# Kernel tuning notes

Hardware: AMD Instinct MI355X
Metric: run time of the kernel (lower is better)

Reference implementation:

```python
import jax, jax.numpy as jnp
import numpy as np

INPUT_DIM = 128
HIDDEN_DIM = 128
WINDOW_SIZE = 256
BLOCK_SIZE = 256
BATCH = 8
SEQ = 8192


def setup_inputs() -> dict:
    key = jax.random.key(0)
    ks = jax.random.split(key, 7)
    s = 1.0 / np.sqrt(INPUT_DIM)
    return {
        "x": jax.random.normal(ks[0], (BATCH, SEQ, INPUT_DIM), dtype=jnp.float32),
        "Wq": jax.random.normal(ks[1], (HIDDEN_DIM, INPUT_DIM), dtype=jnp.float32) * s,
        "bq": jax.random.normal(ks[2], (HIDDEN_DIM,), dtype=jnp.float32) * s,
        "Wk": jax.random.normal(ks[3], (HIDDEN_DIM, INPUT_DIM), dtype=jnp.float32) * s,
        "bk": jax.random.normal(ks[4], (HIDDEN_DIM,), dtype=jnp.float32) * s,
        "Wv": jax.random.normal(ks[5], (HIDDEN_DIM, INPUT_DIM), dtype=jnp.float32) * s,
        "bv": jax.random.normal(ks[6], (HIDDEN_DIM,), dtype=jnp.float32) * s,
    }


def reference(x, Wq, bq, Wk, bk, Wv, bv):
    B, S, D = x.shape
    bs, w = BLOCK_SIZE, WINDOW_SIZE
    nb = S // bs
    halo = w - 1
    W = bs + 2 * halo  # per-block K/V window width

    q = x @ Wq.T + bq  # [B,S,H]
    k = x @ Wk.T + bk
    v = x @ Wv.T + bv

    # Zero-pad K/V by halo on both sides. Since there is NO softmax, padded
    # zero keys give zero scores and padded zero values contribute zero —
    # this exactly reproduces the torch code's clamped window slicing.
    k_pad = jnp.pad(k, ((0, 0), (halo, halo), (0, 0)))
    v_pad = jnp.pad(v, ((0, 0), (halo, halo), (0, 0)))

    # Gather overlapping windows: [B, nb, W, H]
    starts = jnp.arange(nb) * bs  # window start in padded coords
    idx = starts[:, None] + jnp.arange(W)[None, :]  # [nb, W]
    k_win = k_pad[:, idx, :]
    v_win = v_pad[:, idx, :]

    q_blk = q.reshape(B, nb, bs, -1)  # [B, nb, bs, H]

    scale = 1.0 / jnp.sqrt(jnp.float32(D))
    attn = jnp.einsum('bnqh,bnkh->bnqk', q_blk, k_win) * scale  # no softmax
    out = jnp.einsum('bnqk,bnkh->bnqh', attn, v_win)
    return out.reshape(B, S, -1)
```

## Files before the change

kernel.cpp:

```cpp
#include <hip/hip_runtime.h>
#include <stdint.h>


#define B_ 8
#define S_ 8192
#define LDT 68
#define LDG 164
#define LDM 132
#define LDQP 36
#define XTB 21760
#define GOFF 43520
#define SMEMSZ 96000

using bf16x4 = __attribute__((ext_vector_type(4))) short;
using bf16x8 = __attribute__((ext_vector_type(8))) short;
using f32x16 = __attribute__((ext_vector_type(16))) float;

__device__ __forceinline__ short f2bf(float f) {
  union { float f; uint32_t u; } v; v.f = f;
  uint32_t r = v.u + 0x7fffu + ((v.u >> 16) & 1u);
  return (short)(r >> 16);
}

__device__ __forceinline__ bf16x8 cvt8(float4 a, float4 b) {
  bf16x8 r;
  r[0] = f2bf(a.x); r[1] = f2bf(a.y); r[2] = f2bf(a.z); r[3] = f2bf(a.w);
  r[4] = f2bf(b.x); r[5] = f2bf(b.y); r[6] = f2bf(b.z); r[7] = f2bf(b.w);
  return r;
}

__device__ __forceinline__ bf16x8 ld8(const short* p) {
  bf16x4 lo = *(const bf16x4*)p;
  bf16x4 hi = *(const bf16x4*)(p + 4);
  return __builtin_shufflevector(lo, hi, 0, 1, 2, 3, 4, 5, 6, 7);
}

__global__ __launch_bounds__(512, 2) void fused_kernel(
    const float* __restrict__ x,
    const float* __restrict__ Wq, const float* __restrict__ bq,
    const float* __restrict__ Wk, const float* __restrict__ bk,
    const float* __restrict__ Wv, const float* __restrict__ bv,
    float* __restrict__ out)
{
  __shared__ __align__(16) char smem[SMEMSZ];

  const int tid  = threadIdx.x;
  const int lane = tid & 63;
  const int wv   = tid >> 6;
  const int c    = lane & 31;
  const int hl   = lane >> 5;

  const int swz = (blockIdx.x & 7) * 32 + (blockIdx.x >> 3);
  const int b   = swz >> 5;
  const int n   = swz & 31;

  const int win_lo = (n == 0) ? 0 : n * 256 - 255;
  const int win_hi = (n == 31) ? S_ : n * 256 + 511;
  const int jlo    = (n == 0) ? 4 : 0;
  const int jhi    = (n == 31) ? 8 : 12;
  const int cbase  = n * 256 - 256;

  const float* xb = x + (size_t)b * S_ * 128;

  bf16x8 ib[2];
  #pragma unroll
  for (int kst = 0; kst < 2; ++kst)
    #pragma unroll
    for (int j = 0; j < 8; ++j)
      ib[kst][j] = (kst * 16 + hl * 8 + j == c) ? (short)0x3F80 : (short)0;

  const int st = wv >> 2, dt = wv & 3;

  int t0i, t0j, t1i, t1j;
  switch (wv) {
    case 0: t0i=0; t0j=0; t1i=0; t1j=4; break;
    case 1: t0i=1; t0j=1; t1i=1; t1j=4; break;
    case 2: t0i=2; t0j=2; t1i=2; t1j=4; break;
    case 3: t0i=3; t0j=3; t1i=3; t1j=4; break;
    case 4: t0i=0; t0j=1; t1i=4; t1j=4; break;
    case 5: t0i=0; t0j=2; t1i=1; t1j=2; break;
    case 6: t0i=0; t0j=3; t1i=1; t1j=3; break;
    default:t0i=2; t0j=3; t1i=2; t1j=3; break;
  }
  const bool two = (wv != 7);

  {
    int* z0 = (int*)((short*)smem + 129 * LDT);
    int* z1 = (int*)((short*)(smem + XTB) + 129 * LDT);
    for (int i = tid; i < 1054; i += 512) { z0[i] = 0; z1[i] = 0; }
  }

  f32x16 gacc0, gacc1;
  #pragma unroll
  for (int i = 0; i < 16; ++i) { gacc0[i] = 0.f; gacc1[i] = 0.f; }

  auto stageWrite = [&](int c0, short* xt, float4 f0, float4 f1, float4 f2, float4 f3) {
    bf16x8 a0 = cvt8(f0, f1), a1 = cvt8(f2, f3);
    f32x16 cc;
    #pragma unroll
    for (int i = 0; i < 16; ++i) cc[i] = 0.f;
    cc = __builtin_amdgcn_mfma_f32_32x32x16_bf16(a0, ib[0], cc, 0, 0, 0);
    cc = __builtin_amdgcn_mfma_f32_32x32x16_bf16(a1, ib[1], cc, 0, 0, 0);
    const bool mk = (c0 < win_lo) | (c0 + 64 > win_hi);
    short* dst = xt + (dt * 32 + c) * LDT;
    #pragma unroll
    for (int g = 0; g < 4; ++g) {
      #pragma unroll
      for (int p = 0; p < 2; ++p) {
        const int reg = g * 4 + p * 2;
        const int sl  = st * 32 + g * 8 + hl * 4 + p * 2;
        float v0 = cc[reg], v1 = cc[reg + 1];
        if (mk) {
          const int sg = c0 + sl;
          if (sg < win_lo || sg >= win_hi) v0 = 0.f;
          if (sg + 1 < win_lo || sg + 1 >= win_hi) v1 = 0.f;
        }
        const uint32_t pk = (uint32_t)(uint16_t)f2bf(v0) |
                            ((uint32_t)(uint16_t)f2bf(v1) << 16);
        *(uint32_t*)(dst + sl) = pk;
      }
    }
    if (tid < 32) {
      const int s0g = c0 + 2 * tid;
      const uint32_t m0 = (s0g >= win_lo && s0g < win_hi) ? 0x3F80u : 0u;
      const uint32_t m1 = (s0g + 1 >= win_lo && s0g + 1 < win_hi) ? 0x3F80u : 0u;
      *(uint32_t*)(xt + 128 * LDT + 2 * tid) = m0 | (m1 << 16);
    }
  };

  {
    const float* xr = xb + (size_t)(cbase + jlo * 64 + st * 32 + c) * 128 + dt * 32 + hl * 8;
    float4 f0 = ((const float4*)xr)[0], f1 = ((const float4*)xr)[1];
    float4 f2 = *(const float4*)(xr + 16), f3 = *(const float4*)(xr + 20);
    stageWrite(cbase + jlo * 64, (short*)smem, f0, f1, f2, f3);
  }
  __syncthreads();

  for (int j = jlo; j < jhi; ++j) {
    const int jb = (j - jlo) & 1;
    const short* xcur = (const short*)(smem + (size_t)jb * XTB);
    short* xnxt = (short*)(smem + (size_t)(1 - jb) * XTB);
    const bool more = (j + 1 < jhi);

    float4 f0, f1, f2, f3;
    if (more) {
      const float* xr = xb + (size_t)(cbase + (j + 1) * 64 + st * 32 + c) * 128 + dt * 32 + hl * 8;
      f0 = ((const float4*)xr)[0]; f1 = ((const float4*)xr)[1];
      f2 = *(const float4*)(xr + 16); f3 = *(const float4*)(xr + 20);
    }

    #pragma unroll
    for (int kst = 0; kst < 4; ++kst) {
      const int ko = kst * 16 + hl * 8;
      bf16x8 a0 = ld8(xcur + (t0i * 32 + c) * LDT + ko);
      bf16x8 b0 = ld8(xcur + (t0j * 32 + c) * LDT + ko);
      gacc0 = __builtin_amdgcn_mfma_f32_32x32x16_bf16(a0, b0, gacc0, 0, 0, 0);
      bf16x8 a1 = ld8(xcur + (t1i * 32 + c) * LDT + ko);
      bf16x8 b1 = ld8(xcur + (t1j * 32 + c) * LDT + ko);
      gacc1 = __builtin_amdgcn_mfma_f32_32x32x16_bf16(a1, b1, gacc1, 0, 0, 0);
    }

    if (more) stageWrite(cbase + (j + 1) * 64, xnxt, f0, f1, f2, f3);
    __syncthreads();
  }

  short* gl = (short*)(smem + GOFF);
  const float scale = 0.08838834764831845f;

  auto gwrite = [&](f32x16& g, int ti, int tj) {
    #pragma unroll
    for (int reg = 0; reg < 16; ++reg) {
      const int row = ti * 32 + (reg & 3) + 8 * (reg >> 2) + 4 * hl;
      gl[row * LDG + tj * 32 + c] = f2bf(g[reg] * scale);
    }
    if (ti != tj) {
      short* dst = gl + (tj * 32 + c) * LDG + ti * 32;
      #pragma unroll
      for (int g4 = 0; g4 < 4; ++g4) {
        #pragma unroll
        for (int p = 0; p < 2; ++p) {
          const int reg = g4 * 4 + p * 2;
          const int rl  = g4 * 8 + hl * 4 + p * 2;
          const uint32_t pk = (uint32_t)(uint16_t)f2bf(g[reg] * scale) |
                              ((uint32_t)(uint16_t)f2bf(g[reg + 1] * scale) << 16);
          *(uint32_t*)(dst + rl) = pk;
        }
      }
    }
  };
  gwrite(gacc0, t0i, t0j);
  if (two) gwrite(gacc1, t1i, t1j);

  bf16x8 aq[8];
  {
    const float* xr = xb + (size_t)(n * 256 + wv * 32 + c) * 128 + hl * 8;
    #pragma unroll
    for (int kst = 0; kst < 8; ++kst) {
      float4 f0 = *(const float4*)(xr + kst * 16);
      float4 f1 = *(const float4*)(xr + kst * 16 + 4);
      aq[kst] = cvt8(f0, f1);
    }
  }
  __syncthreads();

  short* pl = (short*)smem;
  {
    const int ht = wv & 3;
    const bool lo = (wv < 4);
    const int nd1 = lo ? 3 : 2;
    const int d1b = lo ? 0 : 3;
    const int hr = ht * 32 + c;
    bf16x8 av[9];
    {
      const float* wr = Wv + (size_t)hr * 128 + hl * 8;
      #pragma unroll
      for (int kst = 0; kst < 8; ++kst) {
        float4 f0 = *(const float4*)(wr + kst * 16);
        float4 f1 = *(const float4*)(wr + kst * 16 + 4);
        av[kst] = cvt8(f0, f1);
      }
      bf16x8 a8 = {};
      if (hl == 0) a8[0] = f2bf(bv[hr]);
      av[8] = a8;
    }
    f32x16 pacc[3];
    #pragma unroll
    for (int t = 0; t < 3; ++t)
      #pragma unroll
      for (int i = 0; i < 16; ++i) pacc[t][i] = 0.f;
    #pragma unroll
    for (int t = 0; t < 3; ++t) {
      if (t < nd1) {
        const int d1t = d1b + t;
        #pragma unroll
        for (int kst = 0; kst < 9; ++kst) {
          bf16x8 bb = ld8(gl + (d1t * 32 + c) * LDG + kst * 16 + hl * 8);
          pacc[t] = __builtin_amdgcn_mfma_f32_32x32x16_bf16(av[kst], bb, pacc[t], 0, 0, 0);
        }
      }
    }
    #pragma unroll
    for (int t = 0; t < 3; ++t) {
      if (t < nd1) {
        const int d1t = d1b + t;
        #pragma unroll
        for (int reg = 0; reg < 16; ++reg) {
          const int row = ht * 32 + (reg & 3) + 8 * (reg >> 2) + 4 * hl;
          pl[row * LDG + d1t * 32 + c] = f2bf(pacc[t][reg]);
        }
      }
    }
  }
  __syncthreads();

  short* m_l = gl;
  {
    const int ht = wv >> 1;
    const int dt0 = (wv & 1) * 2;
    bf16x8 ap[9];
    {
      const short* pr = pl + (ht * 32 + c) * LDG + hl * 8;
      #pragma unroll
      for (int kst = 0; kst < 9; ++kst) ap[kst] = ld8(pr + kst * 16);
    }
    f32x16 m2[2];
    #pragma unroll
    for (int t = 0; t < 2; ++t)
      #pragma unroll
      for (int i = 0; i < 16; ++i) m2[t][i] = 0.f;
    #pragma unroll
    for (int t = 0; t < 2; ++t) {
      const int dr = (dt0 + t) * 32 + c;
      const float* wr = Wk + (size_t)dr * 128 + hl * 8;
      #pragma unroll
      for (int kst = 0; kst < 8; ++kst) {
        float4 f0 = *(const float4*)(wr + kst * 16);
        float4 f1 = *(const float4*)(wr + kst * 16 + 4);
        bf16x8 bb = cvt8(f0, f1);
        m2[t] = __builtin_amdgcn_mfma_f32_32x32x16_bf16(ap[kst], bb, m2[t], 0, 0, 0);
      }
      bf16x8 b8 = {};
      if (hl == 0) b8[0] = f2bf(bk[dr]);
      m2[t] = __builtin_amdgcn_mfma_f32_32x32x16_bf16(ap[8], b8, m2[t], 0, 0, 0);
    }
    #pragma unroll
    for (int t = 0; t < 2; ++t) {
      #pragma unroll
      for (int reg = 0; reg < 16; ++reg) {
        const int row = ht * 32 + (reg & 3) + 8 * (reg >> 2) + 4 * hl;
        m_l[row * LDM + (dt0 + t) * 32 + c] = f2bf(m2[t][reg]);
      }
    }
  }
  __syncthreads();

  short* qpat = (short*)(smem + GOFF + 33792) + wv * (32 * LDQP);
  float* opat = (float*)smem + wv * (32 * 36);

  f32x16 oacc[4];
  #pragma unroll
  for (int ht = 0; ht < 4; ++ht)
    #pragma unroll
    for (int i = 0; i < 16; ++i) oacc[ht][i] = 0.f;

  #pragma unroll
  for (int nt = 0; nt < 4; ++nt) {
    bf16x8 wqf[8];
    {
      const float* wr = Wq + (size_t)(nt * 32 + c) * 128 + hl * 8;
      #pragma unroll
      for (int kst = 0; kst < 8; ++kst) {
        float4 f0 = *(const float4*)(wr + kst * 16);
        float4 f1 = *(const float4*)(wr + kst * 16 + 4);
        wqf[kst] = cvt8(f0, f1);
      }
    }
    f32x16 qacc;
    {
      const float bb = bq[nt * 32 + c];
      #pragma unroll
      for (int i = 0; i < 16; ++i) qacc[i] = bb;
    }
    #pragma unroll
    for (int kst = 0; kst < 8; ++kst)
      qacc = __builtin_amdgcn_mfma_f32_32x32x16_bf16(aq[kst], wqf[kst], qacc, 0, 0, 0);
    #pragma unroll
    for (int reg = 0; reg < 16; ++reg) {
      const int row = (reg & 3) + 8 * (reg >> 2) + 4 * hl;
      qpat[row * LDQP + c] = f2bf(qacc[reg]);
    }
    #pragma unroll
    for (int kst2 = 0; kst2 < 2; ++kst2) {
      bf16x8 qf = ld8(qpat + c * LDQP + kst2 * 16 + hl * 8);
      #pragma unroll
      for (int ht = 0; ht < 4; ++ht) {
        bf16x8 bb = ld8(m_l + (ht * 32 + c) * LDM + nt * 32 + kst2 * 16 + hl * 8);
        oacc[ht] = __builtin_amdgcn_mfma_f32_32x32x16_bf16(qf, bb, oacc[ht], 0, 0, 0);
      }
    }
  }

  float* outb = out + ((size_t)b * S_ + n * 256 + wv * 32) * 128;
  #pragma unroll
  for (int ht = 0; ht < 4; ++ht) {
    #pragma unroll
    for (int reg = 0; reg < 16; ++reg) {
      const int row = (reg & 3) + 8 * (reg >> 2) + 4 * hl;
      opat[row * 36 + c] = oacc[ht][reg];
    }
    #pragma unroll
    for (int p = 0; p < 4; ++p) {
      const int row = p * 8 + (lane >> 3);
      float4 vv = *(const float4*)(opat + row * 36 + (lane & 7) * 4);
      *(float4*)(outb + (size_t)row * 128 + ht * 32 + (lane & 7) * 4) = vv;
    }
  }
}

extern "C" void kernel_launch(void* const* d_in, const int* in_sizes, int n_in,
                              void* d_out, int out_size, void* d_ws, size_t ws_size,
                              hipStream_t stream) {
  const float* x  = (const float*)d_in[0];
  const float* Wq = (const float*)d_in[1];
  const float* bq = (const float*)d_in[2];
  const float* Wk = (const float*)d_in[3];
  const float* bk = (const float*)d_in[4];
  const float* Wv = (const float*)d_in[5];
  const float* bv = (const float*)d_in[6];
  float* out = (float*)d_out;

  fused_kernel<<<256, 512, 0, stream>>>(x, Wq, bq, Wk, bk, Wv, bv, out);
}
```

Measured before the change: 139.2 us.

## Load Gram operands directly from global into registers, drop LDS transpose staging

The windowed Gram accumulation (X^T X over the K/V window) no longer transposes x through an identity MFMA into double-buffered LDS tiles. Each wave now loads its column-slice fragments straight from global memory as strided scalar loads, double-buffered in registers. The ones-row statistic is computed from synthesized mask fragments, and the corner count is written analytically. The LDS layout is reorganized and grows, which removes per-chunk barriers and LDS round trips but adds uncoalesced strided global loads, more registers and more shared memory, which may hurt occupancy at two blocks per CU.

```diff
diff --git a/kernel.cpp b/kernel.cpp
--- a/kernel.cpp
+++ b/kernel.cpp
@@ -4,13 +4,12 @@
 
 #define B_ 8
 #define S_ 8192
-#define LDT 68
 #define LDG 164
 #define LDM 132
 #define LDQP 36
-#define XTB 21760
-#define GOFF 43520
-#define SMEMSZ 96000
+#define PLOFF 52480
+#define QPOFF 94464
+#define SMEMSZ 112896
 
 using bf16x4 = __attribute__((ext_vector_type(4))) short;
 using bf16x8 = __attribute__((ext_vector_type(8))) short;
@@ -43,6 +42,7 @@
     float* __restrict__ out)
 {
   __shared__ __align__(16) char smem[SMEMSZ];
+  short* gl = (short*)smem;
 
   const int tid  = threadIdx.x;
   const int lane = tid & 63;
@@ -62,134 +62,142 @@
 
   const float* xb = x + (size_t)b * S_ * 128;
 
-  bf16x8 ib[2];
-  #pragma unroll
-  for (int kst = 0; kst < 2; ++kst)
-    #pragma unroll
-    for (int j = 0; j < 8; ++j)
-      ib[kst][j] = (kst * 16 + hl * 8 + j == c) ? (short)0x3F80 : (short)0;
-
-  const int st = wv >> 2, dt = wv & 3;
-
-  int t0i, t0j, t1i, t1j;
+  {
+    float4 z = {0.f, 0.f, 0.f, 0.f};
+    float4* g4 = (float4*)smem;
+    #pragma unroll
+    for (int i = 0; i < 7; ++i) {
+      int idx = i * 512 + tid;
+      if (idx < 3280) g4[idx] = z;
+    }
+  }
+  __syncthreads();
+
+  int sA, sB, t0i, t0j, t0bs, t1i, t1j, t1as, t1bs;
+  bool hasB, hasT1;
   switch (wv) {
-    case 0: t0i=0; t0j=0; t1i=0; t1j=4; break;
-    case 1: t0i=1; t0j=1; t1i=1; t1j=4; break;
-    case 2: t0i=2; t0j=2; t1i=2; t1j=4; break;
-    case 3: t0i=3; t0j=3; t1i=3; t1j=4; break;
-    case 4: t0i=0; t0j=1; t1i=4; t1j=4; break;
-    case 5: t0i=0; t0j=2; t1i=1; t1j=2; break;
-    case 6: t0i=0; t0j=3; t1i=1; t1j=3; break;
-    default:t0i=2; t0j=3; t1i=2; t1j=3; break;
-  }
-  const bool two = (wv != 7);
-
-  {
-    int* z0 = (int*)((short*)smem + 129 * LDT);
-    int* z1 = (int*)((short*)(smem + XTB) + 129 * LDT);
-    for (int i = tid; i < 1054; i += 512) { z0[i] = 0; z1[i] = 0; }
-  }
+    case 0: sA=0; sB=0; hasB=false; t0i=0; t0j=0; t0bs=0; hasT1=false; t1i=0; t1j=0; t1as=0; t1bs=0; break;
+    case 1: sA=1; sB=2; hasB=true;  t0i=1; t0j=1; t0bs=0; hasT1=true;  t1i=1; t1j=2; t1as=0; t1bs=1; break;
+    case 2: sA=2; sB=3; hasB=true;  t0i=2; t0j=2; t0bs=0; hasT1=true;  t1i=2; t1j=3; t1as=0; t1bs=1; break;
+    case 3: sA=3; sB=0; hasB=true;  t0i=3; t0j=3; t0bs=0; hasT1=true;  t1i=0; t1j=3; t1as=1; t1bs=0; break;
+    case 4: sA=0; sB=2; hasB=true;  t0i=0; t0j=2; t0bs=1; hasT1=true;  t1i=0; t1j=4; t1as=0; t1bs=2; break;
+    case 5: sA=1; sB=3; hasB=true;  t0i=1; t0j=3; t0bs=1; hasT1=true;  t1i=1; t1j=4; t1as=0; t1bs=2; break;
+    case 6: sA=2; sB=3; hasB=true;  t0i=2; t0j=4; t0bs=2; hasT1=true;  t1i=3; t1j=4; t1as=1; t1bs=2; break;
+    default:sA=0; sB=1; hasB=true;  t0i=0; t0j=1; t0bs=1; hasT1=false; t1i=0; t1j=0; t1as=0; t1bs=0; break;
+  }
+  const bool needOnes = (t0bs == 2) || (hasT1 && t1bs == 2);
+
+  auto loadFrags = [&](int c0, bf16x8 (&fr)[2][4]) {
+    const bool mk = (c0 < win_lo) | (c0 + 64 > win_hi);
+    #pragma unroll
+    for (int sl = 0; sl < 2; ++sl) {
+      if (sl == 1 && !hasB) break;
+      const float* base = xb + (size_t)c0 * 128 + ((sl ? sB : sA) * 32 + c) + hl * 8 * 128;
+      #pragma unroll
+      for (int kst = 0; kst < 4; ++kst) {
+        float v[8];
+        #pragma unroll
+        for (int j2 = 0; j2 < 8; ++j2)
+          v[j2] = base[(kst * 16 + j2) * 128];
+        if (mk) {
+          #pragma unroll
+          for (int j2 = 0; j2 < 8; ++j2) {
+            const int sg = c0 + kst * 16 + hl * 8 + j2;
+            if (sg < win_lo || sg >= win_hi) v[j2] = 0.f;
+          }
+        }
+        bf16x8 r;
+        #pragma unroll
+        for (int j2 = 0; j2 < 8; ++j2) r[j2] = f2bf(v[j2]);
+        fr[sl][kst] = r;
+      }
+    }
+  };
+
+  auto onesFrags = [&](int c0, bf16x8 (&ob)[4]) {
+    const bool mk = (c0 < win_lo) | (c0 + 64 > win_hi);
+    #pragma unroll
+    for (int kst = 0; kst < 4; ++kst) {
+      bf16x8 r;
+      #pragma unroll
+      for (int j2 = 0; j2 < 8; ++j2) {
+        const int sg = c0 + kst * 16 + hl * 8 + j2;
+        r[j2] = (!mk || (sg >= win_lo && sg < win_hi)) ? (short)0x3F80 : (short)0;
+      }
+      ob[kst] = r;
+    }
+  };
 
   f32x16 gacc0, gacc1;
   #pragma unroll
   for (int i = 0; i < 16; ++i) { gacc0[i] = 0.f; gacc1[i] = 0.f; }
 
-  auto stageWrite = [&](int c0, short* xt, float4 f0, float4 f1, float4 f2, float4 f3) {
-    bf16x8 a0 = cvt8(f0, f1), a1 = cvt8(f2, f3);
-    f32x16 cc;
-    #pragma unroll
-    for (int i = 0; i < 16; ++i) cc[i] = 0.f;
-    cc = __builtin_amdgcn_mfma_f32_32x32x16_bf16(a0, ib[0], cc, 0, 0, 0);
-    cc = __builtin_amdgcn_mfma_f32_32x32x16_bf16(a1, ib[1], cc, 0, 0, 0);
-    const bool mk = (c0 < win_lo) | (c0 + 64 > win_hi);
-    short* dst = xt + (dt * 32 + c) * LDT;
-    #pragma unroll
-    for (int g = 0; g < 4; ++g) {
-      #pragma unroll
-      for (int p = 0; p < 2; ++p) {
-        const int reg = g * 4 + p * 2;
-        const int sl  = st * 32 + g * 8 + hl * 4 + p * 2;
-        float v0 = cc[reg], v1 = cc[reg + 1];
-        if (mk) {
-          const int sg = c0 + sl;
-          if (sg < win_lo || sg >= win_hi) v0 = 0.f;
-          if (sg + 1 < win_lo || sg + 1 >= win_hi) v1 = 0.f;
-        }
-        const uint32_t pk = (uint32_t)(uint16_t)f2bf(v0) |
-                            ((uint32_t)(uint16_t)f2bf(v1) << 16);
-        *(uint32_t*)(dst + sl) = pk;
-      }
-    }
-    if (tid < 32) {
-      const int s0g = c0 + 2 * tid;
-      const uint32_t m0 = (s0g >= win_lo && s0g < win_hi) ? 0x3F80u : 0u;
-      const uint32_t m1 = (s0g + 1 >= win_lo && s0g + 1 < win_hi) ? 0x3F80u : 0u;
-      *(uint32_t*)(xt + 128 * LDT + 2 * tid) = m0 | (m1 << 16);
+  auto gramChunk = [&](bf16x8 (&fr)[2][4], bf16x8 (&ob)[4]) {
+    #pragma unroll
+    for (int kst = 0; kst < 4; ++kst) {
+      bf16x8 b0 = (t0bs == 0) ? fr[0][kst] : ((t0bs == 1) ? fr[1][kst] : ob[kst]);
+      gacc0 = __builtin_amdgcn_mfma_f32_32x32x16_bf16(fr[0][kst], b0, gacc0, 0, 0, 0);
+      if (hasT1) {
+        bf16x8 a1 = (t1as == 0) ? fr[0][kst] : fr[1][kst];
+        bf16x8 b1 = (t1bs == 0) ? fr[0][kst] : ((t1bs == 1) ? fr[1][kst] : ob[kst]);
+        gacc1 = __builtin_amdgcn_mfma_f32_32x32x16_bf16(a1, b1, gacc1, 0, 0, 0);
+      }
     }
   };
 
-  {
-    const float* xr = xb + (size_t)(cbase + jlo * 64 + st * 32 + c) * 128 + dt * 32 + hl * 8;
-    float4 f0 = ((const float4*)xr)[0], f1 = ((const float4*)xr)[1];
-    float4 f2 = *(const float4*)(xr + 16), f3 = *(const float4*)(xr + 20);
-    stageWrite(cbase + jlo * 64, (short*)smem, f0, f1, f2, f3);
-  }
-  __syncthreads();
-
+  bf16x8 fr0[2][4], fr1[2][4], ob[4];
+  loadFrags(cbase + jlo * 64, fr0);
   for (int j = jlo; j < jhi; ++j) {
-    const int jb = (j - jlo) & 1;
-    const short* xcur = (const short*)(smem + (size_t)jb * XTB);
-    short* xnxt = (short*)(smem + (size_t)(1 - jb) * XTB);
+    const int c0 = cbase + j * 64;
     const bool more = (j + 1 < jhi);
-
-    float4 f0, f1, f2, f3;
-    if (more) {
-      const float* xr = xb + (size_t)(cbase + (j + 1) * 64 + st * 32 + c) * 128 + dt * 32 + hl * 8;
-      f0 = ((const float4*)xr)[0]; f1 = ((const float4*)xr)[1];
-      f2 = *(const float4*)(xr + 16); f3 = *(const float4*)(xr + 20);
-    }
-
-    #pragma unroll
-    for (int kst = 0; kst < 4; ++kst) {
-      const int ko = kst * 16 + hl * 8;
-      bf16x8 a0 = ld8(xcur + (t0i * 32 + c) * LDT + ko);
-      bf16x8 b0 = ld8(xcur + (t0j * 32 + c) * LDT + ko);
-      gacc0 = __builtin_amdgcn_mfma_f32_32x32x16_bf16(a0, b0, gacc0, 0, 0, 0);
-      bf16x8 a1 = ld8(xcur + (t1i * 32 + c) * LDT + ko);
-      bf16x8 b1 = ld8(xcur + (t1j * 32 + c) * LDT + ko);
-      gacc1 = __builtin_amdgcn_mfma_f32_32x32x16_bf16(a1, b1, gacc1, 0, 0, 0);
-    }
-
-    if (more) stageWrite(cbase + (j + 1) * 64, xnxt, f0, f1, f2, f3);
-    __syncthreads();
-  }
-
-  short* gl = (short*)(smem + GOFF);
+    if (needOnes) onesFrags(c0, ob);
+    if (((j - jlo) & 1) == 0) {
+      if (more) loadFrags(c0 + 64, fr1);
+      gramChunk(fr0, ob);
+    } else {
+      if (more) loadFrags(c0 + 64, fr0);
+      gramChunk(fr1, ob);
+    }
+  }
+
   const float scale = 0.08838834764831845f;
-
   auto gwrite = [&](f32x16& g, int ti, int tj) {
-    #pragma unroll
-    for (int reg = 0; reg < 16; ++reg) {
-      const int row = ti * 32 + (reg & 3) + 8 * (reg >> 2) + 4 * hl;
-      gl[row * LDG + tj * 32 + c] = f2bf(g[reg] * scale);
-    }
-    if (ti != tj) {
-      short* dst = gl + (tj * 32 + c) * LDG + ti * 32;
-      #pragma unroll
-      for (int g4 = 0; g4 < 4; ++g4) {
-        #pragma unroll
-        for (int p = 0; p < 2; ++p) {
-          const int reg = g4 * 4 + p * 2;
-          const int rl  = g4 * 8 + hl * 4 + p * 2;
-          const uint32_t pk = (uint32_t)(uint16_t)f2bf(g[reg] * scale) |
-                              ((uint32_t)(uint16_t)f2bf(g[reg + 1] * scale) << 16);
-          *(uint32_t*)(dst + rl) = pk;
+    if (tj == 4) {
+      if (c == 0) {
+        #pragma unroll
+        for (int reg = 0; reg < 16; ++reg) {
+          const int row = ti * 32 + (reg & 3) + 8 * (reg >> 2) + 4 * hl;
+          const short v = f2bf(g[reg] * scale);
+          gl[row * LDG + 128] = v;
+          gl[128 * LDG + row] = v;
+        }
+      }
+    } else {
+      #pragma unroll
+      for (int reg = 0; reg < 16; ++reg) {
+        const int row = ti * 32 + (reg & 3) + 8 * (reg >> 2) + 4 * hl;
+        gl[row * LDG + tj * 32 + c] = f2bf(g[reg] * scale);
+      }
+      if (ti != tj) {
+        short* dst = gl + (tj * 32 + c) * LDG + ti * 32;
+        #pragma unroll
+        for (int g4 = 0; g4 < 4; ++g4) {
+          #pragma unroll
+          for (int p = 0; p < 2; ++p) {
+            const int reg = g4 * 4 + p * 2;
+            const int rl  = g4 * 8 + hl * 4 + p * 2;
+            const uint32_t pk = (uint32_t)(uint16_t)f2bf(g[reg] * scale) |
+                                ((uint32_t)(uint16_t)f2bf(g[reg + 1] * scale) << 16);
+            *(uint32_t*)(dst + rl) = pk;
+          }
         }
       }
     }
   };
   gwrite(gacc0, t0i, t0j);
-  if (two) gwrite(gacc1, t1i, t1j);
+  if (hasT1) gwrite(gacc1, t1i, t1j);
+  if (tid == 0)
+    gl[128 * LDG + 128] = f2bf((float)(win_hi - win_lo) * scale);
 
   bf16x8 aq[8];
   {
@@ -203,7 +211,7 @@
   }
   __syncthreads();
 
-  short* pl = (short*)smem;
+  short* pl = (short*)(smem + PLOFF);
   {
     const int ht = wv & 3;
     const bool lo = (wv < 4);
@@ -294,8 +302,8 @@
   }
   __syncthreads();
 
-  short* qpat = (short*)(smem + GOFF + 33792) + wv * (32 * LDQP);
-  float* opat = (float*)smem + wv * (32 * 36);
+  short* qpat = (short*)(smem + QPOFF) + wv * (32 * LDQP);
+  float* opat = (float*)(smem + PLOFF) + wv * (32 * 36);
 
   f32x16 oacc[4];
   #pragma unroll
```

Measured after the change: 154.4 us. 11.0% more time.
